# Kernel optimization log

Measured on AMD Instinct MI355X. Metric: run time of the kernel, lower is better.

The kernel has to match this reference:

```python
import jax, jax.numpy as jnp
import numpy as np

B, N, D = 8, 4096, 256
K = 8192

def setup_inputs() -> dict:
    key = jax.random.key(0)
    k1, k2 = jax.random.split(key)
    x = jax.random.normal(k1, (B, N, D), dtype=jnp.float32)
    codebook = jax.random.normal(k2, (K, D), dtype=jnp.float32)
    return {"x": x, "codebook": codebook}

def reference(x, codebook):
    """Euclidean VQ forward: cdist + argmin nearest-codebook assignment,
    straight-through quantization, commitment loss, and the scatter-based
    EMA statistics (cluster counts and per-cluster sums)."""
    b, n, d = x.shape
    k = codebook.shape[0]
    flat = x.reshape(-1, d)                                  # [BN, D]
    x2 = jnp.sum(flat * flat, axis=-1, keepdims=True)        # [BN, 1]
    c2 = jnp.sum(codebook * codebook, axis=-1)               # [K]
    dist = x2 + c2[None, :] - 2.0 * (flat @ codebook.T)      # [BN, K]
    embed_ind = jnp.argmin(dist, axis=-1)                    # [BN]
    quantize = codebook[embed_ind].reshape(b, n, d)          # gather
    # commitment loss (codebook detached, as in EMA codebooks)
    commit_loss = jnp.mean((jax.lax.stop_gradient(quantize) - x) ** 2)
    # straight-through estimator
    quantize_st = x + jax.lax.stop_gradient(quantize - x)
    # EMA codebook-update statistics (scatter / segment reductions)
    cluster_size = jax.ops.segment_sum(
        jnp.ones_like(embed_ind, dtype=x.dtype), embed_ind, num_segments=k)  # [K]
    embed_sum = jax.ops.segment_sum(flat, embed_ind, num_segments=k)         # [K, D]
    return quantize_st, embed_ind.reshape(b, n), commit_loss, cluster_size, embed_sum
```

## Files before the change

kernel.cpp:

```cpp
#include <hip/hip_runtime.h>
#include <hip/hip_bf16.h>
#include <math.h>

#define DIM 256
#define KCODES 8192
#define BN_TOTAL 32768
#define NSPLIT 2

#define OUT_IND 8388608
#define OUT_LOSS 8421376
#define OUT_CS 8421377
#define OUT_ES 8429569
#define OUT_TOTAL 10526721

#define XI8_OFF 0
#define CI8_OFF 4194304
#define PART_OFF OUT_ES

typedef unsigned short u16;
typedef unsigned char u8;
typedef unsigned int u32;
typedef __attribute__((ext_vector_type(4))) int i32x4;
typedef __attribute__((address_space(1))) const void gvoid_t;
typedef __attribute__((address_space(3))) void lvoid_t;

#define QSCALE (127.0f / 6.0f)
#define NEG2S2 (-2.0f * (6.0f / 127.0f) * (6.0f / 127.0f))

__global__ __launch_bounds__(256) void vq_prep(const float* __restrict__ x,
                                               const float* __restrict__ cb,
                                               u8* __restrict__ Xi8,
                                               u8* __restrict__ Ci8,
                                               float* __restrict__ c2,
                                               float* __restrict__ c2m) {
  int b = blockIdx.x;
  bool isx = (b < 2048);
  int g = (isx ? b : (b - 2048)) * 256 + threadIdx.x;
  int row = g >> 4;
  int chunk = g & 15;
  const float* src = (isx ? x : cb) + (size_t)row * DIM + chunk * 16;
  float vv[16];
#pragma unroll
  for (int q = 0; q < 4; ++q) {
    float4 v = *(const float4*)(src + q * 4);
    vv[q * 4 + 0] = v.x; vv[q * 4 + 1] = v.y;
    vv[q * 4 + 2] = v.z; vv[q * 4 + 3] = v.w;
  }
  u32 w[4];
  float s = 0.0f;
#pragma unroll
  for (int q = 0; q < 4; ++q) {
    u32 acc = 0;
#pragma unroll
    for (int e = 0; e < 4; ++e) {
      float v = vv[q * 4 + e];
      s += v * v;
      float vs = fminf(fmaxf(v * QSCALE, -127.0f), 127.0f);
      int iv = (int)rintf(vs);
      acc |= ((u32)(u8)(char)iv) << (8 * e);
    }
    w[q] = acc;
  }
  uint4 pk = {w[0], w[1], w[2], w[3]};
  if (isx) {
    *(uint4*)(Xi8 + (size_t)row * DIM + chunk * 16) = pk;
  } else {
    int kbg = chunk >> 2;
    int j = chunk & 3;
    int js = j ^ ((row >> 1) & 3);
    *(uint4*)(Ci8 + (size_t)row * DIM + kbg * 64 + js * 16) = pk;
#pragma unroll
    for (int m = 1; m <= 8; m <<= 1) s += __shfl_xor(s, m, 64);
    if (chunk == 0) { c2[row] = s; c2m[row] = s - 256.0f; }
  }
}

__global__ __launch_bounds__(256, 2)
void vq_mfma(const u8* __restrict__ XB, const u8* __restrict__ CBb,
             const float* __restrict__ c2m, float2* __restrict__ partials) {
  __shared__ __align__(16) u8 As[2][128][64];
  const int t = threadIdx.x;
  const int wid = t >> 6;
  const int lane = t & 63;
  const int lhi = lane >> 4, llo = lane & 15;
  const int sl = lhi ^ ((llo >> 1) & 3);
  const int wm = wid & 1;
  const int wn = wid >> 1;
  const int rt = blockIdx.x & 255;
  const int s = blockIdx.x >> 8;
  const int row0 = rt * 128;
  const int code0base = s * (KCODES / NSPLIT);

  i32x4 b[4][4];
#pragma unroll
  for (int n = 0; n < 4; ++n) {
    const u8* bp = XB + (size_t)(row0 + wn * 64 + n * 16 + llo) * DIM + lhi * 16;
#pragma unroll
    for (int kb = 0; kb < 4; ++kb)
      b[n][kb] = *(const i32x4*)(bp + kb * 64);
  }

  char* AsB = (char*)As;
  const int srow = lane >> 2;
  const int scol = (lane & 3) << 4;

  float v1[4], v2[4], v3[4];
#pragma unroll
  for (int n = 0; n < 4; ++n) { v1[n] = INFINITY; v2[n] = INFINITY; v3[n] = INFINITY; }

  auto STAGE = [&](int ct, int kb, int d) {
#pragma unroll
    for (int i = 0; i < 2; ++i) {
      const int p = wid * 2 + i;
      const int cblk = p * 16;
      const u8* sp = CBb + (size_t)(code0base + ct * 128 + cblk + srow) * DIM +
                     kb * 64 + scol;
      char* dp = AsB + (d << 13) + (p << 10);
      __builtin_amdgcn_global_load_lds((gvoid_t*)sp, (lvoid_t*)dp, 16, 0, 0);
    }
  };

  STAGE(0, 0, 0);

#pragma unroll 1
  for (int ct = 0; ct < 32; ++ct) {
    const int code0 = code0base + ct * 128;
    i32x4 acc[4][4];
#pragma unroll
    for (int m = 0; m < 4; ++m)
#pragma unroll
      for (int n = 0; n < 4; ++n) acc[m][n] = (i32x4){0, 0, 0, 0};

#pragma unroll
    for (int kb = 0; kb < 4; ++kb) {
      const int cc = ct * 4 + kb;
      if (cc < 127) {
        const int nct = (kb == 3) ? ct + 1 : ct;
        const int nkb = (kb == 3) ? 0 : kb + 1;
        STAGE(nct, nkb, (cc + 1) & 1);
      }
      __syncthreads();
      const char* src = AsB + ((cc & 1) << 13);
      i32x4 a[4];
#pragma unroll
      for (int m = 0; m < 4; ++m)
        a[m] = *(const i32x4*)(src + ((wm * 64 + m * 16 + llo) << 6) + (sl << 4));
#pragma unroll
      for (int m = 0; m < 4; ++m)
#pragma unroll
        for (int n = 0; n < 4; ++n)
          acc[m][n] = __builtin_amdgcn_mfma_i32_16x16x64_i8(a[m], b[n][kb],
                                                            acc[m][n], 0, 0, 0);
      if (kb == 3) {
#pragma unroll
        for (int m = 0; m < 4; ++m) {
          int cbase = code0 + wm * 64 + m * 16 + lhi * 4;
          float4 cv = *(const float4*)(c2m + cbase);
          float cvv[4] = {cv.x, cv.y, cv.z, cv.w};
#pragma unroll
          for (int n = 0; n < 4; ++n) {
#pragma unroll
            for (int r = 0; r < 4; ++r) {
              float d = fmaf((float)acc[m][n][r], NEG2S2, cvv[r]);
              float key = __uint_as_float((__float_as_uint(d) & ~0x1FFFu) |
                                          (u32)(cbase + r));
              float ov1 = v1[n], ov2 = v2[n];
              v1[n] = fminf(key, ov1);
              v2[n] = __builtin_amdgcn_fmed3f(key, ov1, v2[n]);
              v3[n] = __builtin_amdgcn_fmed3f(key, ov2, v3[n]);
            }
          }
        }
      }
      __syncthreads();
    }
  }
#pragma unroll
  for (int n = 0; n < 4; ++n) {
    int row = row0 + wn * 64 + n * 16 + llo;
    int slot = s * 8 + wm * 4 + lhi;
    size_t base = ((size_t)row * 16 + slot) * 2;
    partials[base] = make_float2(v1[n], v2[n]);
    partials[base + 1] = make_float2(v3[n], 0.0f);
  }
}

__global__ __launch_bounds__(256)
void vq_pick(const float* __restrict__ x, const float* __restrict__ cb,
             const float* __restrict__ c2g, const float2* __restrict__ partials,
             int* __restrict__ ind, float* __restrict__ out_ind,
             float* __restrict__ out_q, int* __restrict__ cnt,
             float* __restrict__ loss_part) {
  __shared__ float lsm[4];
  int wid = threadIdx.x >> 6, lane = threadIdx.x & 63;
  int row = blockIdx.x * 4 + wid;
  float cv = INFINITY, cv2 = INFINITY, cv3 = INFINITY;
  if (lane < 16) {
    size_t base = ((size_t)row * 16 + lane) * 2;
    float2 a = partials[base];
    float2 bb = partials[base + 1];
    cv = a.x; cv2 = a.y; cv3 = bb.x;
  }
  int cand[4];
#pragma unroll
  for (int rsel = 0; rsel < 4; ++rsel) {
    float bv = cv;
#pragma unroll
    for (int mask = 1; mask < 16; mask <<= 1)
      bv = fminf(bv, __shfl_xor(bv, mask, 64));
    bv = __shfl(bv, 0, 64);
    cand[rsel] = (int)(__float_as_uint(bv) & 8191u);
    if (cv == bv) { cv = cv2; cv2 = cv3; cv3 = INFINITY; }
  }
  const float4 xv = *(const float4*)(x + (size_t)row * DIM + lane * 4);
  float4 q0 = *(const float4*)(cb + (size_t)cand[0] * DIM + lane * 4);
  float4 q1 = *(const float4*)(cb + (size_t)cand[1] * DIM + lane * 4);
  float4 q2 = *(const float4*)(cb + (size_t)cand[2] * DIM + lane * 4);
  float4 q3 = *(const float4*)(cb + (size_t)cand[3] * DIM + lane * 4);
  float d0 = xv.x * q0.x + xv.y * q0.y + xv.z * q0.z + xv.w * q0.w;
  float d1 = xv.x * q1.x + xv.y * q1.y + xv.z * q1.z + xv.w * q1.w;
  float d2 = xv.x * q2.x + xv.y * q2.y + xv.z * q2.z + xv.w * q2.w;
  float d3 = xv.x * q3.x + xv.y * q3.y + xv.z * q3.z + xv.w * q3.w;
  float x2 = xv.x * xv.x + xv.y * xv.y + xv.z * xv.z + xv.w * xv.w;
#pragma unroll
  for (int mask = 1; mask < 64; mask <<= 1) {
    d0 += __shfl_xor(d0, mask, 64);
    d1 += __shfl_xor(d1, mask, 64);
    d2 += __shfl_xor(d2, mask, 64);
    d3 += __shfl_xor(d3, mask, 64);
    x2 += __shfl_xor(x2, mask, 64);
  }
  float e0 = fmaf(-2.0f, d0, c2g[cand[0]]);
  float e1 = fmaf(-2.0f, d1, c2g[cand[1]]);
  float e2 = fmaf(-2.0f, d2, c2g[cand[2]]);
  float e3 = fmaf(-2.0f, d3, c2g[cand[3]]);
  float best = e0; int bk = cand[0];
  if (e1 < best || (e1 == best && cand[1] < bk)) { best = e1; bk = cand[1]; }
  if (e2 < best || (e2 == best && cand[2] < bk)) { best = e2; bk = cand[2]; }
  if (e3 < best || (e3 == best && cand[3] < bk)) { best = e3; bk = cand[3]; }
  float4 q = (bk == cand[1]) ? q1 : (bk == cand[2]) ? q2 : (bk == cand[3]) ? q3 : q0;
  *(float4*)(out_q + (size_t)row * DIM + lane * 4) = q;
  if (lane == 0) {
    ind[row] = bk;
    out_ind[row] = (float)bk;
    atomicAdd(cnt + bk, 1);
    lsm[wid] = x2 + best;
  }
  __syncthreads();
  if (threadIdx.x == 0)
    loss_part[blockIdx.x] = lsm[0] + lsm[1] + lsm[2] + lsm[3];
}

__global__ __launch_bounds__(1024)
void vq_scan(const int* __restrict__ cnt, int* __restrict__ offs,
             int* __restrict__ woffs, float* __restrict__ out_cs,
             const float* __restrict__ loss_part, float* __restrict__ out_loss) {
  __shared__ int ssum[1024];
  __shared__ float sls[1024];
  int tid = threadIdx.x;
  int c[8], loc[8];
  int s = 0;
#pragma unroll
  for (int j = 0; j < 8; ++j) {
    c[j] = cnt[tid * 8 + j];
    loc[j] = s;
    s += c[j];
  }
  ssum[tid] = s;
  float ls = 0.0f;
#pragma unroll
  for (int j = 0; j < 8; ++j) ls += loss_part[tid * 8 + j];
  sls[tid] = ls;
  __syncthreads();
  for (int off = 1; off < 1024; off <<= 1) {
    int v = (tid >= off) ? ssum[tid - off] : 0;
    __syncthreads();
    ssum[tid] += v;
    __syncthreads();
  }
  int base = (tid > 0) ? ssum[tid - 1] : 0;
#pragma unroll
  for (int j = 0; j < 8; ++j) {
    int o = base + loc[j];
    offs[tid * 8 + j] = o;
    woffs[tid * 8 + j] = o;
    out_cs[tid * 8 + j] = (float)c[j];
  }
  for (int off = 512; off >= 1; off >>= 1) {
    if (tid < off) sls[tid] += sls[tid + off];
    __syncthreads();
  }
  if (tid == 0) *out_loss = sls[0] * (1.0f / 8388608.0f);
}

__global__ __launch_bounds__(256)
void vq_scatter(const int* __restrict__ ind, int* __restrict__ woffs,
                int* __restrict__ rowlist) {
  int row = blockIdx.x * 256 + threadIdx.x;
  int k = ind[row];
  int pos = atomicAdd(woffs + k, 1);
  rowlist[pos] = row;
}

__global__ __launch_bounds__(256)
void vq_esum(const float* __restrict__ x, const int* __restrict__ offs,
             const int* __restrict__ cnt, const int* __restrict__ rowlist,
             float* __restrict__ out_es) {
  __shared__ float4 sred[3][64];
  int k = blockIdx.x;
  int wid = threadIdx.x >> 6, lane = threadIdx.x & 63;
  int start = offs[k], n = cnt[k];
  const int* rl = rowlist + start;
  int jb = (n * wid) >> 2, je = (n * (wid + 1)) >> 2;
  float4 acc = {0.f, 0.f, 0.f, 0.f};
  int j = jb;
  for (; j + 4 <= je; j += 4) {
    int r0 = rl[j], r1 = rl[j + 1], r2 = rl[j + 2], r3 = rl[j + 3];
    float4 v0 = *(const float4*)(x + (size_t)r0 * DIM + lane * 4);
    float4 v1 = *(const float4*)(x + (size_t)r1 * DIM + lane * 4);
    float4 v2 = *(const float4*)(x + (size_t)r2 * DIM + lane * 4);
    float4 v3 = *(const float4*)(x + (size_t)r3 * DIM + lane * 4);
    acc.x += v0.x + v1.x + v2.x + v3.x;
    acc.y += v0.y + v1.y + v2.y + v3.y;
    acc.z += v0.z + v1.z + v2.z + v3.z;
    acc.w += v0.w + v1.w + v2.w + v3.w;
  }
  for (; j < je; ++j) {
    int r = rl[j];
    float4 v = *(const float4*)(x + (size_t)r * DIM + lane * 4);
    acc.x += v.x; acc.y += v.y; acc.z += v.z; acc.w += v.w;
  }
  if (wid > 0) sred[wid - 1][lane] = acc;
  __syncthreads();
  if (wid == 0) {
    float4 a1 = sred[0][lane], a2 = sred[1][lane], a3 = sred[2][lane];
    acc.x += a1.x + a2.x + a3.x;
    acc.y += a1.y + a2.y + a3.y;
    acc.z += a1.z + a2.z + a3.z;
    acc.w += a1.w + a2.w + a3.w;
    *(float4*)(out_es + (size_t)k * DIM + lane * 4) = acc;
  }
}

extern "C" void kernel_launch(void* const* d_in, const int* in_sizes, int n_in,
                              void* d_out, int out_size, void* d_ws,
                              size_t ws_size, hipStream_t stream) {
  const float* x = (const float*)d_in[0];
  const float* cb = (const float*)d_in[1];
  float* out = (float*)d_out;
  float* out_q = out;
  float* out_ind = out + OUT_IND;
  float* out_loss = out + OUT_LOSS;
  float* out_cs = out + OUT_CS;
  float* out_es = out + OUT_ES;

  u8* Xi8 = (u8*)(out + XI8_OFF);
  u8* Ci8 = (u8*)(out + CI8_OFF);
  float2* partials = (float2*)(out + PART_OFF);

  char* w = (char*)d_ws;
  int* cnt = (int*)w;
  int* offs = (int*)(w + (32 << 10));
  int* woffs = (int*)(w + (64 << 10));
  float* loss_part = (float*)(w + (96 << 10));
  int* ind = (int*)(w + (128 << 10));
  int* rowlist = (int*)(w + (256 << 10));
  float* c2 = (float*)(w + (384 << 10));
  float* c2m = (float*)(w + (416 << 10));

  hipMemsetAsync(cnt, 0, KCODES * sizeof(int), stream);
  vq_prep<<<2560, 256, 0, stream>>>(x, cb, Xi8, Ci8, c2, c2m);
  vq_mfma<<<256 * NSPLIT, 256, 0, stream>>>(Xi8, Ci8, c2m, partials);
  vq_pick<<<BN_TOTAL / 4, 256, 0, stream>>>(x, cb, c2, partials, ind, out_ind,
                                            out_q, cnt, loss_part);
  vq_scan<<<1, 1024, 0, stream>>>(cnt, offs, woffs, out_cs, loss_part, out_loss);
  vq_scatter<<<BN_TOTAL / 256, 256, 0, stream>>>(ind, woffs, rowlist);
  vq_esum<<<KCODES, 256, 0, stream>>>(x, offs, cnt, rowlist, out_es);
}
```

Measured before the change: 189.6 us.

## Switch VQ distance keys to integer math, halve row tile, keep top-2

The codebook norm term is pre-scaled into integer units, so distance keys come from integer subtraction with the code index packed into the low bits, and selection uses integer min/max instead of float FMA and med3. Each block now covers 64 rows instead of 128, with a top-2 rather than top-3 candidate list per lane. This cuts accumulator and candidate registers enough to raise launch bounds to 4 waves per SIMD, and launches 1024 blocks. The trade-offs are that B fragments are reused across fewer codes per LDS stage, the integer rounding of the norm term adds some error, and fewer candidates go to the exact float re-rank.

```diff
diff --git a/kernel.cpp b/kernel.cpp
--- a/kernel.cpp
+++ b/kernel.cpp
@@ -5,7 +5,6 @@
 #define DIM 256
 #define KCODES 8192
 #define BN_TOTAL 32768
-#define NSPLIT 2
 
 #define OUT_IND 8388608
 #define OUT_LOSS 8421376
@@ -25,14 +24,14 @@
 typedef __attribute__((address_space(3))) void lvoid_t;
 
 #define QSCALE (127.0f / 6.0f)
-#define NEG2S2 (-2.0f * (6.0f / 127.0f) * (6.0f / 127.0f))
+#define INV_2S2 (16129.0f / 72.0f)
 
 __global__ __launch_bounds__(256) void vq_prep(const float* __restrict__ x,
                                                const float* __restrict__ cb,
                                                u8* __restrict__ Xi8,
                                                u8* __restrict__ Ci8,
                                                float* __restrict__ c2,
-                                               float* __restrict__ c2m) {
+                                               int* __restrict__ c2i) {
   int b = blockIdx.x;
   bool isx = (b < 2048);
   int g = (isx ? b : (b - 2048)) * 256 + threadIdx.x;
@@ -71,13 +70,16 @@
     *(uint4*)(Ci8 + (size_t)row * DIM + kbg * 64 + js * 16) = pk;
 #pragma unroll
     for (int m = 1; m <= 8; m <<= 1) s += __shfl_xor(s, m, 64);
-    if (chunk == 0) { c2[row] = s; c2m[row] = s - 256.0f; }
-  }
-}
-
-__global__ __launch_bounds__(256, 2)
+    if (chunk == 0) {
+      c2[row] = s;
+      c2i[row] = (int)rintf((s - 256.0f) * INV_2S2);
+    }
+  }
+}
+
+__global__ __launch_bounds__(256, 4)
 void vq_mfma(const u8* __restrict__ XB, const u8* __restrict__ CBb,
-             const float* __restrict__ c2m, float2* __restrict__ partials) {
+             const int* __restrict__ c2i, int2* __restrict__ partials) {
   __shared__ __align__(16) u8 As[2][128][64];
   const int t = threadIdx.x;
   const int wid = t >> 6;
@@ -86,15 +88,15 @@
   const int sl = lhi ^ ((llo >> 1) & 3);
   const int wm = wid & 1;
   const int wn = wid >> 1;
-  const int rt = blockIdx.x & 255;
-  const int s = blockIdx.x >> 8;
-  const int row0 = rt * 128;
-  const int code0base = s * (KCODES / NSPLIT);
-
-  i32x4 b[4][4];
-#pragma unroll
-  for (int n = 0; n < 4; ++n) {
-    const u8* bp = XB + (size_t)(row0 + wn * 64 + n * 16 + llo) * DIM + lhi * 16;
+  const int rt = blockIdx.x & 511;
+  const int s = blockIdx.x >> 9;
+  const int row0 = rt * 64;
+  const int code0base = s * 4096;
+
+  i32x4 b[2][4];
+#pragma unroll
+  for (int n = 0; n < 2; ++n) {
+    const u8* bp = XB + (size_t)(row0 + wn * 32 + n * 16 + llo) * DIM + lhi * 16;
 #pragma unroll
     for (int kb = 0; kb < 4; ++kb)
       b[n][kb] = *(const i32x4*)(bp + kb * 64);
@@ -104,9 +106,9 @@
   const int srow = lane >> 2;
   const int scol = (lane & 3) << 4;
 
-  float v1[4], v2[4], v3[4];
-#pragma unroll
-  for (int n = 0; n < 4; ++n) { v1[n] = INFINITY; v2[n] = INFINITY; v3[n] = INFINITY; }
+  int v1[2], v2[2];
+#pragma unroll
+  for (int n = 0; n < 2; ++n) { v1[n] = 0x7FFFFFFF; v2[n] = 0x7FFFFFFF; }
 
   auto STAGE = [&](int ct, int kb, int d) {
 #pragma unroll
@@ -125,11 +127,11 @@
 #pragma unroll 1
   for (int ct = 0; ct < 32; ++ct) {
     const int code0 = code0base + ct * 128;
-    i32x4 acc[4][4];
+    i32x4 acc[4][2];
 #pragma unroll
     for (int m = 0; m < 4; ++m)
 #pragma unroll
-      for (int n = 0; n < 4; ++n) acc[m][n] = (i32x4){0, 0, 0, 0};
+      for (int n = 0; n < 2; ++n) acc[m][n] = (i32x4){0, 0, 0, 0};
 
 #pragma unroll
     for (int kb = 0; kb < 4; ++kb) {
@@ -148,26 +150,24 @@
 #pragma unroll
       for (int m = 0; m < 4; ++m)
 #pragma unroll
-        for (int n = 0; n < 4; ++n)
+        for (int n = 0; n < 2; ++n)
           acc[m][n] = __builtin_amdgcn_mfma_i32_16x16x64_i8(a[m], b[n][kb],
                                                             acc[m][n], 0, 0, 0);
       if (kb == 3) {
 #pragma unroll
         for (int m = 0; m < 4; ++m) {
           int cbase = code0 + wm * 64 + m * 16 + lhi * 4;
-          float4 cv = *(const float4*)(c2m + cbase);
-          float cvv[4] = {cv.x, cv.y, cv.z, cv.w};
-#pragma unroll
-          for (int n = 0; n < 4; ++n) {
+          int4 cv = *(const int4*)(c2i + cbase);
+          int cvv[4] = {cv.x, cv.y, cv.z, cv.w};
+#pragma unroll
+          for (int n = 0; n < 2; ++n) {
 #pragma unroll
             for (int r = 0; r < 4; ++r) {
-              float d = fmaf((float)acc[m][n][r], NEG2S2, cvv[r]);
-              float key = __uint_as_float((__float_as_uint(d) & ~0x1FFFu) |
-                                          (u32)(cbase + r));
-              float ov1 = v1[n], ov2 = v2[n];
-              v1[n] = fminf(key, ov1);
-              v2[n] = __builtin_amdgcn_fmed3f(key, ov1, v2[n]);
-              v3[n] = __builtin_amdgcn_fmed3f(key, ov2, v3[n]);
+              int diff = cvv[r] - acc[m][n][r];
+              int key = (int)(((u32)diff << 13) + (u32)(cbase + r));
+              int ov1 = v1[n];
+              v1[n] = min(key, ov1);
+              v2[n] = min(v2[n], max(key, ov1));
             }
           }
         }
@@ -176,41 +176,37 @@
     }
   }
 #pragma unroll
-  for (int n = 0; n < 4; ++n) {
-    int row = row0 + wn * 64 + n * 16 + llo;
+  for (int n = 0; n < 2; ++n) {
+    int row = row0 + wn * 32 + n * 16 + llo;
     int slot = s * 8 + wm * 4 + lhi;
-    size_t base = ((size_t)row * 16 + slot) * 2;
-    partials[base] = make_float2(v1[n], v2[n]);
-    partials[base + 1] = make_float2(v3[n], 0.0f);
+    partials[(size_t)row * 16 + slot] = make_int2(v1[n], v2[n]);
   }
 }
 
 __global__ __launch_bounds__(256)
 void vq_pick(const float* __restrict__ x, const float* __restrict__ cb,
-             const float* __restrict__ c2g, const float2* __restrict__ partials,
+             const float* __restrict__ c2g, const int2* __restrict__ partials,
              int* __restrict__ ind, float* __restrict__ out_ind,
              float* __restrict__ out_q, int* __restrict__ cnt,
              float* __restrict__ loss_part) {
   __shared__ float lsm[4];
   int wid = threadIdx.x >> 6, lane = threadIdx.x & 63;
   int row = blockIdx.x * 4 + wid;
-  float cv = INFINITY, cv2 = INFINITY, cv3 = INFINITY;
+  int cv = 0x7FFFFFFF, cv2 = 0x7FFFFFFF;
   if (lane < 16) {
-    size_t base = ((size_t)row * 16 + lane) * 2;
-    float2 a = partials[base];
-    float2 bb = partials[base + 1];
-    cv = a.x; cv2 = a.y; cv3 = bb.x;
+    int2 p = partials[(size_t)row * 16 + lane];
+    cv = p.x; cv2 = p.y;
   }
   int cand[4];
 #pragma unroll
   for (int rsel = 0; rsel < 4; ++rsel) {
-    float bv = cv;
+    int bv = cv;
 #pragma unroll
     for (int mask = 1; mask < 16; mask <<= 1)
-      bv = fminf(bv, __shfl_xor(bv, mask, 64));
+      bv = min(bv, __shfl_xor(bv, mask, 64));
     bv = __shfl(bv, 0, 64);
-    cand[rsel] = (int)(__float_as_uint(bv) & 8191u);
-    if (cv == bv) { cv = cv2; cv2 = cv3; cv3 = INFINITY; }
+    cand[rsel] = bv & 8191;
+    if (cv == bv) { cv = cv2; cv2 = 0x7FFFFFFF; }
   }
   const float4 xv = *(const float4*)(x + (size_t)row * DIM + lane * 4);
   float4 q0 = *(const float4*)(cb + (size_t)cand[0] * DIM + lane * 4);
@@ -356,7 +352,7 @@
 
   u8* Xi8 = (u8*)(out + XI8_OFF);
   u8* Ci8 = (u8*)(out + CI8_OFF);
-  float2* partials = (float2*)(out + PART_OFF);
+  int2* partials = (int2*)(out + PART_OFF);
 
   char* w = (char*)d_ws;
   int* cnt = (int*)w;
@@ -366,11 +362,11 @@
   int* ind = (int*)(w + (128 << 10));
   int* rowlist = (int*)(w + (256 << 10));
   float* c2 = (float*)(w + (384 << 10));
-  float* c2m = (float*)(w + (416 << 10));
+  int* c2i = (int*)(w + (416 << 10));
 
   hipMemsetAsync(cnt, 0, KCODES * sizeof(int), stream);
-  vq_prep<<<2560, 256, 0, stream>>>(x, cb, Xi8, Ci8, c2, c2m);
-  vq_mfma<<<256 * NSPLIT, 256, 0, stream>>>(Xi8, Ci8, c2m, partials);
+  vq_prep<<<2560, 256, 0, stream>>>(x, cb, Xi8, Ci8, c2, c2i);
+  vq_mfma<<<1024, 256, 0, stream>>>(Xi8, Ci8, c2i, partials);
   vq_pick<<<BN_TOTAL / 4, 256, 0, stream>>>(x, cb, c2, partials, ind, out_ind,
                                             out_q, cnt, loss_part);
   vq_scan<<<1, 1024, 0, stream>>>(cnt, offs, woffs, out_cs, loss_part, out_loss);
```

New measurement: 184.5 us. 2.7% less time.
